# Optimization experiments

Measured on AMD Instinct MI355X. Metric: run time of the kernel, lower is better.

## Reference

```python
import jax, jax.numpy as jnp
import numpy as np

B, S, T, H, V = 32, 64, 64, 512, 32000


def setup_inputs() -> dict:
    key = jax.random.key(0)
    ks = jax.random.split(key, 14)
    enc = jax.random.normal(ks[0], (B, S, H), jnp.float32)
    h0 = jax.random.normal(ks[1], (1, B, H), jnp.float32)
    # encoder padding mask: at least half of each row valid (avoids all -inf rows)
    src_len = jax.random.randint(ks[2], (B,), S // 2, S + 1)
    enc_mask = (jnp.arange(S)[None, :] < src_len[:, None])
    tgt = jax.random.randint(ks[3], (B, T), 0, V)
    fra_len = jax.random.randint(ks[4], (B,), 1, T + 1).at[0].set(T)
    s = 1.0 / np.sqrt(H)
    emb = jax.random.normal(ks[5], (V, H), jnp.float32) * s
    W_ih = jax.random.uniform(ks[6], (3 * H, H), jnp.float32, -s, s)
    W_hh = jax.random.uniform(ks[7], (3 * H, H), jnp.float32, -s, s)
    b_ih = jax.random.uniform(ks[8], (3 * H,), jnp.float32, -s, s)
    b_hh = jax.random.uniform(ks[9], (3 * H,), jnp.float32, -s, s)
    W_cc = jax.random.uniform(ks[10], (H, 2 * H), jnp.float32, -s, s)
    b_cc = jnp.zeros((H,), jnp.float32)
    W_out = jax.random.uniform(ks[11], (V, H), jnp.float32, -s, s)
    b_out = jnp.zeros((V,), jnp.float32)
    return {"all_encoder_hidden_states": enc, "initial_decoder_hidden_state": h0,
            "encoder_output_mask": enc_mask, "target_input": tgt, "fra_length": fra_len,
            "embedding": emb, "W_ih": W_ih, "W_hh": W_hh, "b_ih": b_ih, "b_hh": b_hh,
            "W_cc": W_cc, "b_cc": b_cc, "W_out": W_out, "b_out": b_out}


def reference(all_encoder_hidden_states, initial_decoder_hidden_state, encoder_output_mask,
              target_input, fra_length, embedding, W_ih, W_hh, b_ih, b_hh,
              W_cc, b_cc, W_out, b_out):
    enc = all_encoder_hidden_states            # [B,S,H]
    mask = encoder_output_mask                 # [B,S] bool
    xs = embedding[target_input].transpose(1, 0, 2)  # [T,B,H]
    ts = jnp.arange(xs.shape[0])

    def step(h, inp):                          # h: [B,H]
        x, t = inp
        gx = x @ W_ih.T + b_ih                 # [B,3H]
        gh = h @ W_hh.T + b_hh
        gxr, gxz, gxn = jnp.split(gx, 3, axis=-1)
        ghr, ghz, ghn = jnp.split(gh, 3, axis=-1)
        r = jax.nn.sigmoid(gxr + ghr)
        z = jax.nn.sigmoid(gxz + ghz)
        n = jnp.tanh(gxn + r * ghn)
        h_new = (1.0 - z) * n + z * h          # torch GRU update
        # Luong dot-product attention
        scores = jnp.einsum('bsh,bh->bs', enc, h_new)
        scores = jnp.where(mask, scores, -jnp.inf)
        alphas = jax.nn.softmax(scores, axis=-1)
        ctx = jnp.einsum('bs,bsh->bh', alphas, enc)
        ho = jnp.tanh(jnp.concatenate([ctx, h_new], axis=-1) @ W_cc.T + b_cc)
        logit = ho @ W_out.T + b_out           # [B,V]
        active = (t < fra_length)[:, None]
        h_next = jnp.where(active, h_new, h)   # freeze finished sequences
        return h_next, logit

    _, logits = jax.lax.scan(step, initial_decoder_hidden_state[0], (xs, ts))
    logits = logits.transpose(1, 0, 2)          # [B,T,V]
    return jax.nn.log_softmax(logits, axis=-1)
```

## Files before the change

### kernel.cpp

```cpp
#include <hip/hip_runtime.h>

static constexpr int Bn = 32, Sn = 64, Tn = 64, Hn = 512, Vn = 32000;
static constexpr int H3 = 1536;

typedef __attribute__((ext_vector_type(8))) short bf16x8;
typedef __attribute__((ext_vector_type(4))) float f32x4;

__device__ __forceinline__ short f2bf(float f) {
    unsigned u = __float_as_uint(f);
    u += 0x7FFFu + ((u >> 16) & 1u);
    return (short)(u >> 16);
}
__device__ __forceinline__ float bf2f(short s) {
    return __uint_as_float(((unsigned)(unsigned short)s) << 16);
}

__device__ __forceinline__ void gload16(const void* g, void* l) {
    __builtin_amdgcn_global_load_lds(
        (const __attribute__((address_space(1))) unsigned int*)g,
        (__attribute__((address_space(3))) unsigned int*)l, 16, 0, 0);
}

__global__ __launch_bounds__(128) void k_gather(const int* __restrict__ tgt,
                                                const float* __restrict__ emb,
                                                short* __restrict__ Xb) {
    int m = blockIdx.x;
    int c = threadIdx.x * 4;
    const float4 v = *(const float4*)(emb + (long)tgt[m] * Hn + c);
    short4 o; o.x = f2bf(v.x); o.y = f2bf(v.y); o.z = f2bf(v.z); o.w = f2bf(v.w);
    *(short4*)(Xb + (long)m * Hn + c) = o;
}

__global__ __launch_bounds__(256) void k_cvt_flat(const float* __restrict__ src,
                                                  short* __restrict__ dst, long n4) {
    long i = (long)blockIdx.x * 256 + threadIdx.x;
    if (i >= n4) return;
    const float4 v = *(const float4*)(src + i * 4);
    short4 o; o.x = f2bf(v.x); o.y = f2bf(v.y); o.z = f2bf(v.z); o.w = f2bf(v.w);
    *(short4*)(dst + i * 4) = o;
}

__global__ __launch_bounds__(256) void k_cvtW(const float* __restrict__ W_ih,
                                              const float* __restrict__ W_hh,
                                              const float* __restrict__ W_cc,
                                              short* __restrict__ Wih_b, short* __restrict__ Whh_b,
                                              short* __restrict__ Wc1_b, short* __restrict__ Wc2_b) {
    long u = (long)blockIdx.x * 256 + threadIdx.x;
    const float* src; short* dst;
    if (u < 196608)       { long e = u * 4;            src = W_ih + e; dst = Wih_b + e; }
    else if (u < 393216)  { long e = (u - 196608) * 4; src = W_hh + e; dst = Whh_b + e; }
    else if (u < 458752)  { long e = (u - 393216) * 4; long r = e >> 9; int c = (int)(e & 511);
                            src = W_cc + r * 1024 + c;       dst = Wc1_b + e; }
    else                  { long e = (u - 458752) * 4; long r = e >> 9; int c = (int)(e & 511);
                            src = W_cc + r * 1024 + 512 + c; dst = Wc2_b + e; }
    const float4 v = *(const float4*)src;
    short4 o; o.x = f2bf(v.x); o.y = f2bf(v.y); o.z = f2bf(v.z); o.w = f2bf(v.w);
    *(short4*)dst = o;
}

__global__ __launch_bounds__(256) void k_gemm_bf16(const short* __restrict__ A, int lda,
                                                   const short* __restrict__ Bm, int ldb,
                                                   const float* __restrict__ bias,
                                                   float* __restrict__ C, int ldc, int K) {
    __shared__ short lA[4096];
    __shared__ short lB[4096];
    const int tid = threadIdx.x;
    const int row0 = blockIdx.y * 128;
    const int col0 = blockIdx.x * 128;
    const int lane = tid & 63;
    const int w = tid >> 6;
    const int wr = w >> 1, wc = w & 1;
    const int g = lane >> 4, rr = lane & 15;

    f32x4 acc[4][4];
    for (int m = 0; m < 4; ++m)
        for (int n = 0; n < 4; ++n)
            for (int q = 0; q < 4; ++q) acc[m][n][q] = 0.f;

    for (int kk = 0; kk < K; kk += 32) {
        for (int p = 0; p < 2; ++p) {
            int u = p * 256 + tid;
            int kg = u >> 7, r = u & 127;
            gload16(A + (long)(row0 + r) * lda + kk + kg * 8, &lA[u * 8]);
            gload16(Bm + (long)(col0 + r) * ldb + kk + kg * 8, &lB[u * 8]);
        }
        __syncthreads();
        bf16x8 av[4], bv[4];
        for (int m = 0; m < 4; ++m)
            av[m] = *(const bf16x8*)&lA[(g * 128 + wr * 64 + m * 16 + rr) * 8];
        for (int n = 0; n < 4; ++n)
            bv[n] = *(const bf16x8*)&lB[(g * 128 + wc * 64 + n * 16 + rr) * 8];
        for (int m = 0; m < 4; ++m)
            for (int n = 0; n < 4; ++n)
                acc[m][n] = __builtin_amdgcn_mfma_f32_16x16x32_bf16(av[m], bv[n], acc[m][n], 0, 0, 0);
        __syncthreads();
    }

    for (int n = 0; n < 4; ++n) {
        int gc = col0 + wc * 64 + n * 16 + rr;
        float bb = bias ? bias[gc] : 0.f;
        for (int m = 0; m < 4; ++m) {
            int gr = row0 + wr * 64 + m * 16 + g * 4;
            for (int q = 0; q < 4; ++q)
                C[(long)(gr + q) * ldc + gc] = acc[m][n][q] + bb;
        }
    }
}

__global__ __launch_bounds__(256) void k_gemm_logits(const short* __restrict__ A,
                                                     const short* __restrict__ Bm,
                                                     const float* __restrict__ bias,
                                                     float* __restrict__ C,
                                                     float* __restrict__ stats) {
    __shared__ short lA[4096];
    __shared__ short lB[4096];
    __shared__ float sml[128][2];
    __shared__ float ssl[128][2];
    const int tid = threadIdx.x;
    const int row0 = blockIdx.y * 128;
    const int col0 = blockIdx.x * 128;
    const int lane = tid & 63;
    const int w = tid >> 6;
    const int wr = w >> 1, wc = w & 1;
    const int g = lane >> 4, rr = lane & 15;

    f32x4 acc[4][4];
    for (int m = 0; m < 4; ++m)
        for (int n = 0; n < 4; ++n)
            for (int q = 0; q < 4; ++q) acc[m][n][q] = 0.f;

    for (int kk = 0; kk < 512; kk += 32) {
        for (int p = 0; p < 2; ++p) {
            int u = p * 256 + tid;
            int kg = u >> 7, r = u & 127;
            gload16(A + (long)(row0 + r) * 512 + kk + kg * 8, &lA[u * 8]);
            gload16(Bm + (long)(col0 + r) * 512 + kk + kg * 8, &lB[u * 8]);
        }
        __syncthreads();
        bf16x8 av[4], bv[4];
        for (int m = 0; m < 4; ++m)
            av[m] = *(const bf16x8*)&lA[(g * 128 + wr * 64 + m * 16 + rr) * 8];
        for (int n = 0; n < 4; ++n)
            bv[n] = *(const bf16x8*)&lB[(g * 128 + wc * 64 + n * 16 + rr) * 8];
        for (int m = 0; m < 4; ++m)
            for (int n = 0; n < 4; ++n)
                acc[m][n] = __builtin_amdgcn_mfma_f32_16x16x32_bf16(av[m], bv[n], acc[m][n], 0, 0, 0);
        __syncthreads();
    }

    float bb[4];
    #pragma unroll
    for (int n = 0; n < 4; ++n) bb[n] = bias[col0 + wc * 64 + n * 16 + rr];

    #pragma unroll
    for (int n = 0; n < 4; ++n) {
        int gc = col0 + wc * 64 + n * 16 + rr;
        #pragma unroll
        for (int m = 0; m < 4; ++m) {
            int gr = row0 + wr * 64 + m * 16 + g * 4;
            #pragma unroll
            for (int q = 0; q < 4; ++q)
                C[(long)(gr + q) * Vn + gc] = acc[m][n][q] + bb[n];
        }
    }
    #pragma unroll
    for (int m = 0; m < 4; ++m) {
        #pragma unroll
        for (int q = 0; q < 4; ++q) {
            float mx = acc[m][0][q] + bb[0];
            mx = fmaxf(mx, acc[m][1][q] + bb[1]);
            mx = fmaxf(mx, acc[m][2][q] + bb[2]);
            mx = fmaxf(mx, acc[m][3][q] + bb[3]);
            mx = fmaxf(mx, __shfl_xor(mx, 1));
            mx = fmaxf(mx, __shfl_xor(mx, 2));
            mx = fmaxf(mx, __shfl_xor(mx, 4));
            mx = fmaxf(mx, __shfl_xor(mx, 8));
            float s = __expf(acc[m][0][q] + bb[0] - mx) + __expf(acc[m][1][q] + bb[1] - mx)
                    + __expf(acc[m][2][q] + bb[2] - mx) + __expf(acc[m][3][q] + bb[3] - mx);
            s += __shfl_xor(s, 1);
            s += __shfl_xor(s, 2);
            s += __shfl_xor(s, 4);
            s += __shfl_xor(s, 8);
            if (rr == 0) {
                const int r = wr * 64 + m * 16 + g * 4 + q;
                sml[r][wc] = mx; ssl[r][wc] = s;
            }
        }
    }
    __syncthreads();
    if (tid < 128) {
        const float m0 = sml[tid][0], m1 = sml[tid][1];
        const float mm = fmaxf(m0, m1);
        const float ss = ssl[tid][0] * __expf(m0 - mm) + ssl[tid][1] * __expf(m1 - mm);
        float2* sp = (float2*)stats;
        sp[(long)(row0 + tid) * 256 + blockIdx.x] = make_float2(mm, ss);
    }
}

__global__ __launch_bounds__(256) void k_sub(float* __restrict__ out, const float* __restrict__ stats) {
    const long row = blockIdx.x;
    const int tid = threadIdx.x;
    __shared__ float lse_s;
    if (tid < 64) {
        float m = -__builtin_inff(), s = 0.f;
        for (int tc = tid; tc < 250; tc += 64) {
            const float2 p = ((const float2*)stats)[row * 256 + tc];
            const float nm = fmaxf(m, p.x);
            s = s * __expf(m - nm) + p.y * __expf(p.x - nm);
            m = nm;
        }
        for (int o = 1; o < 64; o <<= 1) {
            const float om = __shfl_xor(m, o), os = __shfl_xor(s, o);
            const float nm = fmaxf(m, om);
            s = s * __expf(m - nm) + os * __expf(om - nm);
            m = nm;
        }
        if (tid == 0) lse_s = m + logf(s);
    }
    __syncthreads();
    const float lse = lse_s;
    float* p = out + row * (long)Vn;
    for (int i = tid; i < Vn / 4; i += 256) {
        float4 v = *(const float4*)(p + i * 4);
        v.x -= lse; v.y -= lse; v.z -= lse; v.w -= lse;
        *(float4*)(p + i * 4) = v;
    }
}

__global__ __launch_bounds__(256) void k_ho(const short* __restrict__ A1, const short* __restrict__ A2,
                                            const short* __restrict__ B1, const short* __restrict__ B2,
                                            const float* __restrict__ bias, short* __restrict__ C) {
    __shared__ short lA[4096];
    __shared__ short lB[4096];
    const int tid = threadIdx.x;
    const int row0 = blockIdx.y * 128;
    const int col0 = blockIdx.x * 128;
    const int lane = tid & 63;
    const int w = tid >> 6;
    const int wr = w >> 1, wc = w & 1;
    const int g = lane >> 4, rr = lane & 15;

    f32x4 acc[4][4];
    for (int m = 0; m < 4; ++m)
        for (int n = 0; n < 4; ++n)
            for (int q = 0; q < 4; ++q) acc[m][n][q] = 0.f;

    for (int ph = 0; ph < 2; ++ph) {
        const short* A = ph ? A2 : A1;
        const short* Bm = ph ? B2 : B1;
        for (int kk = 0; kk < 512; kk += 32) {
            for (int p = 0; p < 2; ++p) {
                int u = p * 256 + tid;
                int kg = u >> 7, r = u & 127;
                gload16(A + (long)(row0 + r) * 512 + kk + kg * 8, &lA[u * 8]);
                gload16(Bm + (long)(col0 + r) * 512 + kk + kg * 8, &lB[u * 8]);
            }
            __syncthreads();
            bf16x8 av[4], bv[4];
            for (int m = 0; m < 4; ++m)
                av[m] = *(const bf16x8*)&lA[(g * 128 + wr * 64 + m * 16 + rr) * 8];
            for (int n = 0; n < 4; ++n)
                bv[n] = *(const bf16x8*)&lB[(g * 128 + wc * 64 + n * 16 + rr) * 8];
            for (int m = 0; m < 4; ++m)
                for (int n = 0; n < 4; ++n)
                    acc[m][n] = __builtin_amdgcn_mfma_f32_16x16x32_bf16(av[m], bv[n], acc[m][n], 0, 0, 0);
            __syncthreads();
        }
    }

    for (int n = 0; n < 4; ++n) {
        int gc = col0 + wc * 64 + n * 16 + rr;
        float bb = bias[gc];
        for (int m = 0; m < 4; ++m) {
            int gr = row0 + wr * 64 + m * 16 + g * 4;
            for (int q = 0; q < 4; ++q)
                C[(long)(gr + q) * 512 + gc] = f2bf(tanhf(acc[m][n][q] + bb));
        }
    }
}

__device__ __forceinline__ void sig_flag(unsigned* slot, unsigned val) {
    asm volatile("s_waitcnt vmcnt(0)" ::: "memory");
    __syncthreads();
    if (threadIdx.x == 0)
        __hip_atomic_store(slot, val, __ATOMIC_RELAXED, __HIP_MEMORY_SCOPE_AGENT);
}

__global__ __launch_bounds__(512, 1) void k_seq(
    const float* __restrict__ GX, const int* __restrict__ fra,
    const float* __restrict__ h0,
    const short* __restrict__ Whh_b, const float* __restrict__ b_hh,
    short* __restrict__ hn_all,
    unsigned long long* __restrict__ hn_pub,
    unsigned* __restrict__ flags)
{
    __shared__ __align__(16) short h_all[Bn * Hn];
    __shared__ float gh_sl[3 * 16 * 32];
    const int bid = blockIdx.x;
    const int tid = threadIdx.x;
    const int wv = tid >> 6, lane = tid & 63;

    bf16x8 afr[16];
    if (wv < 6) {
        const int g = wv >> 1;
        const int row = g * 512 + bid * 16 + (lane & 15);
        #pragma unroll
        for (int k = 0; k < 16; ++k)
            afr[k] = *(const bf16x8*)(Whh_b + (long)row * 512 + k * 32 + (lane >> 4) * 8);
    }
    #pragma unroll
    for (int it = 0; it < 8; ++it) {
        const int idx2 = it * 512 + tid;
        const int b = idx2 >> 7, ci2 = idx2 & 127;
        const int j0 = ci2 * 4;
        const int soff = b * 512 + ((((ci2 >> 1)) ^ (b & 7)) << 3) + (ci2 & 1) * 4;
        const float4 v = *(const float4*)(h0 + b * 512 + j0);
        unsigned long long pk = (unsigned long long)(unsigned short)f2bf(v.x)
                              | ((unsigned long long)(unsigned short)f2bf(v.y) << 16)
                              | ((unsigned long long)(unsigned short)f2bf(v.z) << 32)
                              | ((unsigned long long)(unsigned short)f2bf(v.w) << 48);
        *(unsigned long long*)&h_all[soff] = pk;
    }

    const int eb = tid >> 4, jj = tid & 15;
    float h_carry = h0[eb * 512 + bid * 16 + jj];
    const int flen_e = fra[eb];

    const int ci2s = wv * 16 + (lane & 15);
    const unsigned* fp = flags + (ci2s >> 2) * 32;
    const int bbase = lane >> 4;

    for (int t = 0; t < Tn; ++t) {
        const long base = (long)(eb * Tn + t) * H3 + bid * 16 + jj;
        const float gxr = GX[base];
        const float gxz = GX[base + 512];
        const float gxn = GX[base + 1024];
        if (t >= 1) {
            while (__hip_atomic_load(fp, __ATOMIC_RELAXED, __HIP_MEMORY_SCOPE_AGENT) < (unsigned)t)
                __builtin_amdgcn_s_sleep(1);
            const unsigned long long* src = hn_pub + ((t - 1) & 1) * 4096;
            #pragma unroll
            for (int it = 0; it < 8; ++it) {
                const int b = bbase + it * 4;
                const unsigned long long v =
                    __hip_atomic_load(src + b * 128 + ci2s, __ATOMIC_RELAXED, __HIP_MEMORY_SCOPE_AGENT);
                const int soff = b * 512 + ((((ci2s >> 1)) ^ (b & 7)) << 3) + (ci2s & 1) * 4;
                *(unsigned long long*)&h_all[soff] = v;
            }
        }
        __syncthreads();
        if (wv < 6) {
            const int g = wv >> 1, n = wv & 1;
            const int bq = n * 16 + (lane & 15);
            f32x4 a0 = {0.f, 0.f, 0.f, 0.f}, a1 = {0.f, 0.f, 0.f, 0.f};
            #pragma unroll
            for (int k = 0; k < 8; ++k) {
                const int c0 = k * 4 + (lane >> 4);
                const int c1 = (k + 8) * 4 + (lane >> 4);
                bf16x8 b0 = *(const bf16x8*)&h_all[bq * 512 + ((c0 ^ (bq & 7)) << 3)];
                bf16x8 b1 = *(const bf16x8*)&h_all[bq * 512 + ((c1 ^ (bq & 7)) << 3)];
                a0 = __builtin_amdgcn_mfma_f32_16x16x32_bf16(afr[k], b0, a0, 0, 0, 0);
                a1 = __builtin_amdgcn_mfma_f32_16x16x32_bf16(afr[k + 8], b1, a1, 0, 0, 0);
            }
            const int r0 = (lane >> 4) * 4;
            #pragma unroll
            for (int q = 0; q < 4; ++q)
                gh_sl[g * 512 + (r0 + q) * 32 + bq] = a0[q] + a1[q];
        }
        __syncthreads();
        {
            const int j = bid * 16 + jj;
            const float ghr = gh_sl[jj * 32 + eb]          + b_hh[j];
            const float ghz = gh_sl[512 + jj * 32 + eb]    + b_hh[512 + j];
            const float ghn = gh_sl[1024 + jj * 32 + eb]   + b_hh[1024 + j];
            const float r = 1.f / (1.f + __expf(-(gxr + ghr)));
            const float z = 1.f / (1.f + __expf(-(gxz + ghz)));
            const float nn = tanhf(gxn + r * ghn);
            const float hv = (1.f - z) * nn + z * h_carry;
            h_carry = (t < flen_e) ? hv : h_carry;
            int w32 = (int)(unsigned short)f2bf(h_carry);
            int n1 = __shfl_down(w32, 1);
            int n2 = __shfl_down(w32, 2);
            int n3 = __shfl_down(w32, 3);
            if ((jj & 3) == 0) {
                unsigned long long pk = (unsigned long long)(unsigned)(w32 | (n1 << 16))
                                      | ((unsigned long long)(unsigned)(n2 | (n3 << 16)) << 32);
                __hip_atomic_store(hn_pub + (t & 1) * 4096 + eb * 128 + bid * 4 + (jj >> 2), pk,
                                   __ATOMIC_RELAXED, __HIP_MEMORY_SCOPE_AGENT);
            }
            sig_flag(flags + bid * 32, (unsigned)(t + 1));
            hn_all[(long)(eb * Tn + t) * Hn + bid * 16 + jj] = f2bf(hv);
        }
    }
}

__global__ __launch_bounds__(512, 1) void k_attn(
    const float* __restrict__ enc, const short* __restrict__ hn_all,
    const void* __restrict__ maskp, short* __restrict__ ctx_b)
{
    __shared__ __align__(16) short encl[64 * 536];
    __shared__ __align__(16) short hnlbuf[64 * 536];
    __shared__ __align__(16) float scl[64 * 64];
    __shared__ __align__(16) short albc[64 * 72];
    const int b = blockIdx.x;
    const int tid = threadIdx.x;
    const int wv = tid >> 6, lane = tid & 63;
    const int g = lane >> 4, rr = lane & 15;

    const unsigned w0 = ((const unsigned*)maskp)[0];
    const int mmode = (w0 == 1u) ? 0 : (w0 == 0x3F800000u ? 2 : 1);

    {
        const float* encb = enc + (long)b * (Sn * Hn);
        #pragma unroll
        for (int it = 0; it < 16; ++it) {
            int e = (it * 512 + tid) * 4;
            float4 v = *(const float4*)(encb + e);
            int s = e >> 9, k = e & 511;
            short4 o; o.x = f2bf(v.x); o.y = f2bf(v.y); o.z = f2bf(v.z); o.w = f2bf(v.w);
            *(short4*)(encl + s * 536 + k) = o;
        }
    }
    {
        const short* hb = hn_all + (long)b * (Tn * Hn);
        #pragma unroll
        for (int it = 0; it < 8; ++it) {
            int u = it * 512 + tid;
            int t = u >> 6, k8 = (u & 63) * 8;
            *(int4*)(hnlbuf + t * 536 + k8) = *(const int4*)(hb + t * 512 + k8);
        }
    }
    __syncthreads();

    for (int i = 0; i < 2; ++i) {
        const int id = wv * 2 + i;
        const int tt = id >> 2, ss = id & 3;
        f32x4 a0 = {0.f, 0.f, 0.f, 0.f}, a1 = {0.f, 0.f, 0.f, 0.f};
        #pragma unroll
        for (int k = 0; k < 8; ++k) {
            bf16x8 av0 = *(const bf16x8*)&hnlbuf[(tt * 16 + rr) * 536 + k * 32 + g * 8];
            bf16x8 bv0 = *(const bf16x8*)&encl[(ss * 16 + rr) * 536 + k * 32 + g * 8];
            bf16x8 av1 = *(const bf16x8*)&hnlbuf[(tt * 16 + rr) * 536 + (k + 8) * 32 + g * 8];
            bf16x8 bv1 = *(const bf16x8*)&encl[(ss * 16 + rr) * 536 + (k + 8) * 32 + g * 8];
            a0 = __builtin_amdgcn_mfma_f32_16x16x32_bf16(av0, bv0, a0, 0, 0, 0);
            a1 = __builtin_amdgcn_mfma_f32_16x16x32_bf16(av1, bv1, a1, 0, 0, 0);
        }
        #pragma unroll
        for (int q = 0; q < 4; ++q)
            scl[(tt * 16 + g * 4 + q) * 64 + ss * 16 + rr] = a0[q] + a1[q];
    }
    __syncthreads();

    {
        const int t = wv * 8 + (lane >> 3);
        const int sub = lane & 7;
        float v[8];
        #pragma unroll
        for (int e = 0; e < 8; ++e) {
            const int s = sub * 8 + e;
            bool mv;
            if (mmode == 0)      mv = ((const int*)maskp)[b * Sn + s] != 0;
            else if (mmode == 1) mv = ((const unsigned char*)maskp)[b * Sn + s] != 0;
            else                 mv = ((const float*)maskp)[b * Sn + s] != 0.f;
            v[e] = mv ? scl[t * 64 + s] : -__builtin_inff();
        }
        float mx = v[0];
        #pragma unroll
        for (int e = 1; e < 8; ++e) mx = fmaxf(mx, v[e]);
        mx = fmaxf(mx, __shfl_xor(mx, 1));
        mx = fmaxf(mx, __shfl_xor(mx, 2));
        mx = fmaxf(mx, __shfl_xor(mx, 4));
        float su = 0.f;
        float ev[8];
        #pragma unroll
        for (int e = 0; e < 8; ++e) { ev[e] = __expf(v[e] - mx); su += ev[e]; }
        su += __shfl_xor(su, 1);
        su += __shfl_xor(su, 2);
        su += __shfl_xor(su, 4);
        const float inv = 1.f / su;
        bf16x8 o;
        #pragma unroll
        for (int e = 0; e < 8; ++e) o[e] = f2bf(ev[e] * inv);
        *(bf16x8*)&albc[t * 72 + sub * 8] = o;
    }
    {
        short* enct = hnlbuf;
        const int j = tid;
        #pragma unroll
        for (int c = 0; c < 8; ++c) {
            bf16x8 tmp;
            #pragma unroll
            for (int e = 0; e < 8; ++e) tmp[e] = encl[(c * 8 + e) * 536 + j];
            *(bf16x8*)&enct[j * 64 + ((c ^ (j & 7)) * 8)] = tmp;
        }
    }
    __syncthreads();

    {
        const short* enct = hnlbuf;
        for (int i = 0; i < 16; ++i) {
            const int id = wv * 16 + i;
            const int tt = id >> 5, jt = id & 31;
            const int jr = jt * 16 + rr;
            f32x4 acc = {0.f, 0.f, 0.f, 0.f};
            #pragma unroll
            for (int kk = 0; kk < 2; ++kk) {
                bf16x8 av = *(const bf16x8*)&albc[(tt * 16 + rr) * 72 + kk * 32 + g * 8];
                const int c = kk * 4 + g;
                bf16x8 bv = *(const bf16x8*)&enct[jr * 64 + ((c ^ (jr & 7)) * 8)];
                acc = __builtin_amdgcn_mfma_f32_16x16x32_bf16(av, bv, acc, 0, 0, 0);
            }
            #pragma unroll
            for (int q = 0; q < 4; ++q) {
                const int t = tt * 16 + g * 4 + q;
                ctx_b[(long)(b * Tn + t) * Hn + jr] = f2bf(acc[q]);
            }
        }
    }
}

extern "C" void kernel_launch(void* const* d_in, const int* in_sizes, int n_in,
                              void* d_out, int out_size, void* d_ws, size_t ws_size,
                              hipStream_t stream) {
    const float* enc   = (const float*)d_in[0];
    const float* h0    = (const float*)d_in[1];
    const void*  maskp = d_in[2];
    const int*   tgt   = (const int*)d_in[3];
    const int*   fra   = (const int*)d_in[4];
    const float* emb   = (const float*)d_in[5];
    const float* W_ih  = (const float*)d_in[6];
    const float* W_hh  = (const float*)d_in[7];
    const float* b_ih  = (const float*)d_in[8];
    const float* b_hh  = (const float*)d_in[9];
    const float* W_cc  = (const float*)d_in[10];
    const float* b_cc  = (const float*)d_in[11];
    const float* W_out = (const float*)d_in[12];
    const float* b_out = (const float*)d_in[13];
    float* out = (float*)d_out;

    char* ws = (char*)d_ws;
    float*    GX      = (float*)ws;   ws += (long)2048 * 1536 * 4;
    short*    Xb      = (short*)ws;   ws += (long)2048 * 512 * 2;
    short*    Wih_b   = (short*)ws;   ws += (long)1536 * 512 * 2;
    short*    Wout_b  = (short*)ws;   ws += (long)32000 * 512 * 2;
    short*    Whh_b   = (short*)ws;   ws += (long)1536 * 512 * 2;
    short*    Wc1_b   = (short*)ws;   ws += (long)512 * 512 * 2;
    short*    Wcc2_b  = (short*)ws;   ws += (long)512 * 512 * 2;
    short*    ho_b    = (short*)ws;   ws += (long)2048 * 512 * 2;
    short*    hn_all  = (short*)ws;   ws += (long)2048 * 512 * 2;
    short*    ctx_b   = (short*)ws;   ws += (long)2048 * 512 * 2;
    float*    stats   = (float*)ws;   ws += (long)2048 * 256 * 2 * 4;
    unsigned long long* hn_pub = (unsigned long long*)ws; ws += (long)2 * 4096 * 8;
    unsigned* flags   = (unsigned*)ws; ws += 1024 * 4;

    hipMemsetAsync(flags, 0, 1024 * 4, stream);
    k_gather<<<2048, 128, 0, stream>>>(tgt, emb, Xb);
    k_cvtW<<<2048, 256, 0, stream>>>(W_ih, W_hh, W_cc, Wih_b, Whh_b, Wc1_b, Wcc2_b);
    k_cvt_flat<<<16000, 256, 0, stream>>>(W_out, Wout_b, (long)32000 * 512 / 4);

    k_gemm_bf16<<<dim3(12, 16), 256, 0, stream>>>(Xb, 512, Wih_b, 512, b_ih, GX, 1536, 512);

    k_seq<<<32, 512, 0, stream>>>(GX, fra, h0, Whh_b, b_hh, hn_all, hn_pub, flags);

    k_attn<<<32, 512, 0, stream>>>(enc, hn_all, maskp, ctx_b);

    k_ho<<<dim3(4, 16), 256, 0, stream>>>(ctx_b, hn_all, Wc1_b, Wcc2_b, b_cc, ho_b);

    k_gemm_logits<<<dim3(250, 16), 256, 0, stream>>>(ho_b, Wout_b, b_out, out, stats);

    k_sub<<<2048, 256, 0, stream>>>(out, stats);
}
```

Measured before the change: 716.3 us.

## Overlap W_out conversion with recurrence, merge prep kernels, stage logits in bf16

Merges the embedding gather and small weight conversions into one prep kernel. The W_out fp32-to-bf16 conversion moves into extra blocks of the sequential GRU kernel, so it can run on idle CUs while the 32 recurrence blocks work. When workspace allows, the logits GEMM writes bf16 logits to a scratch buffer instead of fp32 to the output, and the final kernel reads them back, which cuts one fp32 read of the output. GRU biases are hoisted out of the time loop. The risks are bf16 rounding of logits before the log-softmax subtraction, and that the extra blocks could compete with or delay the latency-bound recurrence if its spin-wait assumes co-residency.

Result: faster. 675.1 us (-5.8%).

```diff
diff --git a/kernel.cpp b/kernel.cpp
--- a/kernel.cpp
+++ b/kernel.cpp
@@ -21,41 +21,34 @@
         (__attribute__((address_space(3))) unsigned int*)l, 16, 0, 0);
 }
 
-__global__ __launch_bounds__(128) void k_gather(const int* __restrict__ tgt,
-                                                const float* __restrict__ emb,
-                                                short* __restrict__ Xb) {
-    int m = blockIdx.x;
-    int c = threadIdx.x * 4;
-    const float4 v = *(const float4*)(emb + (long)tgt[m] * Hn + c);
-    short4 o; o.x = f2bf(v.x); o.y = f2bf(v.y); o.z = f2bf(v.z); o.w = f2bf(v.w);
-    *(short4*)(Xb + (long)m * Hn + c) = o;
-}
-
-__global__ __launch_bounds__(256) void k_cvt_flat(const float* __restrict__ src,
-                                                  short* __restrict__ dst, long n4) {
-    long i = (long)blockIdx.x * 256 + threadIdx.x;
-    if (i >= n4) return;
-    const float4 v = *(const float4*)(src + i * 4);
-    short4 o; o.x = f2bf(v.x); o.y = f2bf(v.y); o.z = f2bf(v.z); o.w = f2bf(v.w);
-    *(short4*)(dst + i * 4) = o;
-}
-
-__global__ __launch_bounds__(256) void k_cvtW(const float* __restrict__ W_ih,
+__global__ __launch_bounds__(256) void k_prep(const int* __restrict__ tgt,
+                                              const float* __restrict__ emb,
+                                              const float* __restrict__ W_ih,
                                               const float* __restrict__ W_hh,
                                               const float* __restrict__ W_cc,
+                                              short* __restrict__ Xb,
                                               short* __restrict__ Wih_b, short* __restrict__ Whh_b,
                                               short* __restrict__ Wc1_b, short* __restrict__ Wc2_b) {
-    long u = (long)blockIdx.x * 256 + threadIdx.x;
-    const float* src; short* dst;
-    if (u < 196608)       { long e = u * 4;            src = W_ih + e; dst = Wih_b + e; }
-    else if (u < 393216)  { long e = (u - 196608) * 4; src = W_hh + e; dst = Whh_b + e; }
-    else if (u < 458752)  { long e = (u - 393216) * 4; long r = e >> 9; int c = (int)(e & 511);
-                            src = W_cc + r * 1024 + c;       dst = Wc1_b + e; }
-    else                  { long e = (u - 458752) * 4; long r = e >> 9; int c = (int)(e & 511);
-                            src = W_cc + r * 1024 + 512 + c; dst = Wc2_b + e; }
-    const float4 v = *(const float4*)src;
-    short4 o; o.x = f2bf(v.x); o.y = f2bf(v.y); o.z = f2bf(v.z); o.w = f2bf(v.w);
-    *(short4*)dst = o;
+    const int bid = blockIdx.x, tid = threadIdx.x;
+    if (bid < 2048) {
+        long u = (long)bid * 256 + tid;
+        const float* src; short* dst;
+        if (u < 196608)       { long e = u * 4;            src = W_ih + e; dst = Wih_b + e; }
+        else if (u < 393216)  { long e = (u - 196608) * 4; src = W_hh + e; dst = Whh_b + e; }
+        else if (u < 458752)  { long e = (u - 393216) * 4; long r = e >> 9; int c = (int)(e & 511);
+                                src = W_cc + r * 1024 + c;       dst = Wc1_b + e; }
+        else                  { long e = (u - 458752) * 4; long r = e >> 9; int c = (int)(e & 511);
+                                src = W_cc + r * 1024 + 512 + c; dst = Wc2_b + e; }
+        const float4 v = *(const float4*)src;
+        short4 o; o.x = f2bf(v.x); o.y = f2bf(v.y); o.z = f2bf(v.z); o.w = f2bf(v.w);
+        *(short4*)dst = o;
+    } else {
+        const int m = (bid - 2048) * 2 + (tid >> 7);
+        const int c = (tid & 127) * 4;
+        const float4 v = *(const float4*)(emb + (long)tgt[m] * Hn + c);
+        short4 o; o.x = f2bf(v.x); o.y = f2bf(v.y); o.z = f2bf(v.z); o.w = f2bf(v.w);
+        *(short4*)(Xb + (long)m * Hn + c) = o;
+    }
 }
 
 __global__ __launch_bounds__(256) void k_gemm_bf16(const short* __restrict__ A, int lda,
@@ -110,8 +103,10 @@
 __global__ __launch_bounds__(256) void k_gemm_logits(const short* __restrict__ A,
                                                      const short* __restrict__ Bm,
                                                      const float* __restrict__ bias,
-                                                     float* __restrict__ C,
-                                                     float* __restrict__ stats) {
+                                                     float* __restrict__ Cf,
+                                                     short* __restrict__ Cb,
+                                                     float* __restrict__ stats,
+                                                     int use_bf16) {
     __shared__ short lA[4096];
     __shared__ short lB[4096];
     __shared__ float sml[128][2];
@@ -152,15 +147,29 @@
     #pragma unroll
     for (int n = 0; n < 4; ++n) bb[n] = bias[col0 + wc * 64 + n * 16 + rr];
 
-    #pragma unroll
-    for (int n = 0; n < 4; ++n) {
-        int gc = col0 + wc * 64 + n * 16 + rr;
-        #pragma unroll
-        for (int m = 0; m < 4; ++m) {
-            int gr = row0 + wr * 64 + m * 16 + g * 4;
-            #pragma unroll
-            for (int q = 0; q < 4; ++q)
-                C[(long)(gr + q) * Vn + gc] = acc[m][n][q] + bb[n];
+    if (use_bf16) {
+        #pragma unroll
+        for (int n = 0; n < 4; ++n) {
+            int gc = col0 + wc * 64 + n * 16 + rr;
+            #pragma unroll
+            for (int m = 0; m < 4; ++m) {
+                int gr = row0 + wr * 64 + m * 16 + g * 4;
+                #pragma unroll
+                for (int q = 0; q < 4; ++q)
+                    Cb[(long)(gr + q) * Vn + gc] = f2bf(acc[m][n][q] + bb[n]);
+            }
+        }
+    } else {
+        #pragma unroll
+        for (int n = 0; n < 4; ++n) {
+            int gc = col0 + wc * 64 + n * 16 + rr;
+            #pragma unroll
+            for (int m = 0; m < 4; ++m) {
+                int gr = row0 + wr * 64 + m * 16 + g * 4;
+                #pragma unroll
+                for (int q = 0; q < 4; ++q)
+                    Cf[(long)(gr + q) * Vn + gc] = acc[m][n][q] + bb[n];
+            }
         }
     }
     #pragma unroll
@@ -197,7 +206,8 @@
     }
 }
 
-__global__ __launch_bounds__(256) void k_sub(float* __restrict__ out, const float* __restrict__ stats) {
+__global__ __launch_bounds__(256) void k_sub(float* __restrict__ out, const short* __restrict__ Cb,
+                                             const float* __restrict__ stats, int use_bf16) {
     const long row = blockIdx.x;
     const int tid = threadIdx.x;
     __shared__ float lse_s;
@@ -220,10 +230,21 @@
     __syncthreads();
     const float lse = lse_s;
     float* p = out + row * (long)Vn;
-    for (int i = tid; i < Vn / 4; i += 256) {
-        float4 v = *(const float4*)(p + i * 4);
-        v.x -= lse; v.y -= lse; v.z -= lse; v.w -= lse;
-        *(float4*)(p + i * 4) = v;
+    if (use_bf16) {
+        const short* cp = Cb + row * (long)Vn;
+        for (int i = tid; i < Vn / 4; i += 256) {
+            short4 c = *(const short4*)(cp + i * 4);
+            float4 v;
+            v.x = bf2f(c.x) - lse; v.y = bf2f(c.y) - lse;
+            v.z = bf2f(c.z) - lse; v.w = bf2f(c.w) - lse;
+            *(float4*)(p + i * 4) = v;
+        }
+    } else {
+        for (int i = tid; i < Vn / 4; i += 256) {
+            float4 v = *(const float4*)(p + i * 4);
+            v.x -= lse; v.y -= lse; v.z -= lse; v.w -= lse;
+            *(float4*)(p + i * 4) = v;
+        }
     }
 }
 
@@ -292,14 +313,29 @@
     const short* __restrict__ Whh_b, const float* __restrict__ b_hh,
     short* __restrict__ hn_all,
     unsigned long long* __restrict__ hn_pub,
-    unsigned* __restrict__ flags)
+    unsigned* __restrict__ flags,
+    const float* __restrict__ W_out, short* __restrict__ Wout_b)
 {
     __shared__ __align__(16) short h_all[Bn * Hn];
     __shared__ float gh_sl[3 * 16 * 32];
     const int bid = blockIdx.x;
     const int tid = threadIdx.x;
+
+    if (bid >= Bn) {
+        const long base = (long)(bid - Bn) * (512 * 16);
+        #pragma unroll
+        for (int it = 0; it < 16; ++it) {
+            long i = base + it * 512 + tid;
+            if (i < (long)Vn * Hn / 4) {
+                const float4 v = *(const float4*)(W_out + i * 4);
+                short4 o; o.x = f2bf(v.x); o.y = f2bf(v.y); o.z = f2bf(v.z); o.w = f2bf(v.w);
+                *(short4*)(Wout_b + i * 4) = o;
+            }
+        }
+        return;
+    }
+
     const int wv = tid >> 6, lane = tid & 63;
-
     bf16x8 afr[16];
     if (wv < 6) {
         const int g = wv >> 1;
@@ -325,13 +361,17 @@
     const int eb = tid >> 4, jj = tid & 15;
     float h_carry = h0[eb * 512 + bid * 16 + jj];
     const int flen_e = fra[eb];
+    const int jglob = bid * 16 + jj;
+    const float bhr = b_hh[jglob];
+    const float bhz = b_hh[512 + jglob];
+    const float bhn = b_hh[1024 + jglob];
 
     const int ci2s = wv * 16 + (lane & 15);
     const unsigned* fp = flags + (ci2s >> 2) * 32;
     const int bbase = lane >> 4;
 
     for (int t = 0; t < Tn; ++t) {
-        const long base = (long)(eb * Tn + t) * H3 + bid * 16 + jj;
+        const long base = (long)(eb * Tn + t) * H3 + jglob;
         const float gxr = GX[base];
         const float gxz = GX[base + 512];
         const float gxn = GX[base + 1024];
@@ -369,10 +409,9 @@
         }
         __syncthreads();
         {
-            const int j = bid * 16 + jj;
-            const float ghr = gh_sl[jj * 32 + eb]          + b_hh[j];
-            const float ghz = gh_sl[512 + jj * 32 + eb]    + b_hh[512 + j];
-            const float ghn = gh_sl[1024 + jj * 32 + eb]   + b_hh[1024 + j];
+            const float ghr = gh_sl[jj * 32 + eb]          + bhr;
+            const float ghz = gh_sl[512 + jj * 32 + eb]    + bhz;
+            const float ghn = gh_sl[1024 + jj * 32 + eb]   + bhn;
             const float r = 1.f / (1.f + __expf(-(gxr + ghr)));
             const float z = 1.f / (1.f + __expf(-(gxz + ghz)));
             const float nn = tanhf(gxn + r * ghn);
@@ -389,7 +428,7 @@
                                    __ATOMIC_RELAXED, __HIP_MEMORY_SCOPE_AGENT);
             }
             sig_flag(flags + bid * 32, (unsigned)(t + 1));
-            hn_all[(long)(eb * Tn + t) * Hn + bid * 16 + jj] = f2bf(hv);
+            hn_all[(long)(eb * Tn + t) * Hn + jglob] = f2bf(hv);
         }
     }
 }
@@ -552,21 +591,23 @@
     float*    stats   = (float*)ws;   ws += (long)2048 * 256 * 2 * 4;
     unsigned long long* hn_pub = (unsigned long long*)ws; ws += (long)2 * 4096 * 8;
     unsigned* flags   = (unsigned*)ws; ws += 1024 * 4;
+    const long cb_bytes = (long)2048 * Vn * 2;
+    const long used = (long)(ws - (char*)d_ws);
+    const int use_bf16 = (ws_size >= (size_t)(used + cb_bytes)) ? 1 : 0;
+    short* Cb = use_bf16 ? (short*)ws : nullptr;
 
     hipMemsetAsync(flags, 0, 1024 * 4, stream);
-    k_gather<<<2048, 128, 0, stream>>>(tgt, emb, Xb);
-    k_cvtW<<<2048, 256, 0, stream>>>(W_ih, W_hh, W_cc, Wih_b, Whh_b, Wc1_b, Wcc2_b);
-    k_cvt_flat<<<16000, 256, 0, stream>>>(W_out, Wout_b, (long)32000 * 512 / 4);
+    k_prep<<<3072, 256, 0, stream>>>(tgt, emb, W_ih, W_hh, W_cc, Xb, Wih_b, Whh_b, Wc1_b, Wcc2_b);
 
     k_gemm_bf16<<<dim3(12, 16), 256, 0, stream>>>(Xb, 512, Wih_b, 512, b_ih, GX, 1536, 512);
 
-    k_seq<<<32, 512, 0, stream>>>(GX, fra, h0, Whh_b, b_hh, hn_all, hn_pub, flags);
+    k_seq<<<544, 512, 0, stream>>>(GX, fra, h0, Whh_b, b_hh, hn_all, hn_pub, flags, W_out, Wout_b);
 
     k_attn<<<32, 512, 0, stream>>>(enc, hn_all, maskp, ctx_b);
 
     k_ho<<<dim3(4, 16), 256, 0, stream>>>(ctx_b, hn_all, Wc1_b, Wcc2_b, b_cc, ho_b);
 
-    k_gemm_logits<<<dim3(250, 16), 256, 0, stream>>>(ho_b, Wout_b, b_out, out, stats);
-
-    k_sub<<<2048, 256, 0, stream>>>(out, stats);
-}
+    k_gemm_logits<<<dim3(250, 16), 256, 0, stream>>>(ho_b, Wout_b, b_out, out, Cb, stats, use_bf16);
+
+    k_sub<<<2048, 256, 0, stream>>>(out, Cb, stats, use_bf16);
+}
```
